# Performance work log

Measured on AMD Instinct MI355X. Metric: run time of the kernel, lower is better.

## Reference

```python
import jax, jax.numpy as jnp
import numpy as np
from jax import lax

RSM_K = 35
PFM_K = 31


def _box_sum(x, k):
    # Separable zero-padded box sum, equivalent to conv2d with a uniform kxk
    # kernel and padding=k//2 (odd k -> SAME). x: [B,1,H,W]
    p = k // 2
    pad = ((0, 0), (0, 0), (p, p), (0, 0))
    x = lax.reduce_window(x, 0.0, lax.add, (1, 1, k, 1), (1, 1, 1, 1), pad)
    pad = ((0, 0), (0, 0), (0, 0), (p, p))
    x = lax.reduce_window(x, 0.0, lax.add, (1, 1, 1, k), (1, 1, 1, 1), pad)
    return x


def _dilate(x, k):
    # Separable morphological dilation == max_pool2d(kernel=k, stride=1, pad=k//2).
    # -inf padding matches torch's max_pool2d padding semantics for 0/1 masks.
    p = k // 2
    ninf = -jnp.inf
    pad = ((0, 0), (0, 0), (p, p), (0, 0))
    x = lax.reduce_window(x, ninf, lax.max, (1, 1, k, 1), (1, 1, 1, 1), pad)
    pad = ((0, 0), (0, 0), (0, 0), (p, p))
    x = lax.reduce_window(x, ninf, lax.max, (1, 1, 1, k), (1, 1, 1, 1), pad)
    return x


def setup_inputs() -> dict:
    key = jax.random.key(0)
    # Sparse binary lesion mask, values exactly 0.0 / 1.0, shape [B,1,H,W]
    masks = (jax.random.uniform(key, (32, 1, 768, 768)) < 0.02).astype(jnp.float32)
    return {"masks": masks}


def reference(masks):
    # RSM: probability map = uniform 35x35 box average (conv2d with 1/k^2 kernel)
    rsm = _box_sum(masks, RSM_K) * (1.0 / (RSM_K * RSM_K))  # [B,1,H,W]
    # PFM: 1 = lesion, 0 = surrounding (inside 31x31 dilation), 2 = ignore
    dilated = _dilate(masks, PFM_K)
    pfm = jnp.where(masks > 0.5, 1, jnp.where(dilated > 0.5, 0, 2))
    pfm = pfm.astype(jnp.int32)[:, 0, :, :]  # [B,H,W]
    return rsm, pfm
```

## Files before the change

kernel.cpp:

```cpp
#include <hip/hip_runtime.h>


#define BATCH 32
#define HH 768
#define WW 768
#define NPIX (HH * WW)

constexpr int TYO  = 48;
constexpr int HALO = 17;
constexpr int ROWS = TYO + 2 * HALO;
constexpr int NSEG = 12;
constexpr int SSEG = NSEG + 2;
constexpr int NT   = 768;
constexpr int NG   = 4;
constexpr int RPG  = TYO / NG;
constexpr int CT   = 192;

typedef float v4f __attribute__((ext_vector_type(4)));

__global__ __launch_bounds__(NT)
void label_gen_fused(const float* __restrict__ in, float* __restrict__ out) {
    __shared__ unsigned long long sbits[ROWS][SSEG];
    __shared__ unsigned int hm[ROWS][CT];

    const int tid  = threadIdx.x;
    const int lane = tid & 63;
    const int wv   = tid >> 6;
    const int y0   = blockIdx.x * TYO;
    const int b    = blockIdx.y;
    const float* __restrict__ src = in + (size_t)b * NPIX;

    for (int lr = wv; lr < ROWS; lr += NT / 64) {
        const int r = y0 - HALO + lr;
        unsigned long long bb[NSEG];
        if ((unsigned)r < (unsigned)HH) {
            const float* rp = src + (size_t)r * WW;
            #pragma unroll
            for (int j = 0; j < NSEG; ++j)
                bb[j] = __ballot(rp[64 * j + lane] > 0.5f);
        } else {
            #pragma unroll
            for (int j = 0; j < NSEG; ++j) bb[j] = 0ull;
        }
        if (lane == 0) {
            sbits[lr][0] = 0ull;
            #pragma unroll
            for (int j = 0; j < NSEG; ++j) sbits[lr][j + 1] = bb[j];
            sbits[lr][SSEG - 1] = 0ull;
        }
    }
    __syncthreads();

    {
        const int r0 = tid / CT;
        const int ct = tid - r0 * CT;
        const int c0 = 4 * ct;
        const int s  = c0 - HALO;
        const int q  = (s >> 6) + 1;
        const int sh = s & 63;
        const unsigned long long M35 = (1ull << 35) - 1;
        for (int lr = r0; lr < ROWS; lr += NG) {
            const unsigned long long w =
                (sbits[lr][q] >> sh) | (sbits[lr][q + 1] << (64 - sh));
            const int h0 = (int)__popcll(w & M35);
            const int h1 = h0 + (int)((w >> 35) & 1) - (int)(w & 1);
            const int h2 = h1 + (int)((w >> 36) & 1) - (int)((w >> 1) & 1);
            const int h3 = h2 + (int)((w >> 37) & 1) - (int)((w >> 2) & 1);
            unsigned long long sm = w | (w >> 1);
            sm |= sm >> 2; sm |= sm >> 4; sm |= sm >> 8;
            const unsigned int o4 = (unsigned int)(((sm >> 2) | (sm >> 17)) & 0xFull);
            const unsigned int m4 = (unsigned int)((w >> 17) & 0xFull);
            const unsigned int mb =
                (((m4 & 1u) | ((m4 & 2u) << 7) | ((m4 & 4u) << 14) | ((m4 & 8u) << 21)) << 6);
            const unsigned int ob =
                (((o4 & 1u) | ((o4 & 2u) << 7) | ((o4 & 4u) << 14) | ((o4 & 8u) << 21)) << 7);
            hm[lr][ct] = (unsigned)h0 | ((unsigned)h1 << 8) | ((unsigned)h2 << 16)
                       | ((unsigned)h3 << 24) | mb | ob;
        }
    }
    __syncthreads();

    const int g   = tid / CT;
    const int ct  = tid - g * CT;
    const int c0  = 4 * ct;
    const int yb  = y0 + RPG * g;
    const int lr0 = RPG * g;

    const unsigned int M6 = 0x003F003Fu;
    const unsigned int M1 = 0x01010101u;

    unsigned int vA = 0, vB = 0;
    unsigned int c31 = 0;
    unsigned int ring_e[2], ring_l[2];
    #pragma unroll
    for (int k = 0; k < 35; ++k) {
        const unsigned int x = hm[lr0 + k][ct];
        vA += x & M6;
        vB += (x >> 8) & M6;
        if (k >= 2 && k <= 32) c31 += (x >> 7) & M1;
        if (k == 0)  ring_l[0] = x;
        if (k == 1)  ring_l[1] = x;
        if (k == 33) ring_e[0] = x;
        if (k == 34) ring_e[1] = x;
    }

    float* orow = out + (size_t)b * NPIX + (size_t)yb * WW + c0;
    float* prow = orow + (size_t)BATCH * NPIX;

    for (int i = 0; i < RPG; ++i) {
        const int lr = lr0 + HALO + i;
        const unsigned int xc = hm[lr][ct];

        v4f r4, p4;
        r4.x = (float)(vA & 0xFFFFu) * (1.0f / 1225.0f);
        r4.y = (float)(vB & 0xFFFFu) * (1.0f / 1225.0f);
        r4.z = (float)(vA >> 16)     * (1.0f / 1225.0f);
        r4.w = (float)(vB >> 16)     * (1.0f / 1225.0f);
        p4.x = ((xc >> 6) & 1u)  ? 1.0f : ((c31 & 0xFFu)         ? 0.0f : 2.0f);
        p4.y = ((xc >> 14) & 1u) ? 1.0f : (((c31 >> 8) & 0xFFu)  ? 0.0f : 2.0f);
        p4.z = ((xc >> 22) & 1u) ? 1.0f : (((c31 >> 16) & 0xFFu) ? 0.0f : 2.0f);
        p4.w = ((xc >> 30) & 1u) ? 1.0f : ((c31 >> 24)           ? 0.0f : 2.0f);

        __builtin_nontemporal_store(r4, (v4f*)orow);
        __builtin_nontemporal_store(p4, (v4f*)prow);
        orow += WW; prow += WW;

        if (i < RPG - 1) {
            const unsigned int xe   = hm[lr + 18][ct];
            const unsigned int xl31 = hm[lr0 + 2 + i][ct];
            const unsigned int xe31 = ring_e[i & 1];
            const unsigned int xl   = ring_l[i & 1];
            ring_e[i & 1] = xe;
            ring_l[i & 1] = xl31;
            vA  = (vA + (xe & M6)) - (xl & M6);
            vB  = (vB + ((xe >> 8) & M6)) - ((xl >> 8) & M6);
            c31 = (c31 + ((xe31 >> 7) & M1)) - ((xl31 >> 7) & M1);
        }
    }
}

extern "C" void kernel_launch(void* const* d_in, const int* in_sizes, int n_in,
                              void* d_out, int out_size, void* d_ws, size_t ws_size,
                              hipStream_t stream) {
    const float* masks = (const float*)d_in[0];
    float* out = (float*)d_out;
    dim3 grid(HH / TYO, BATCH);
    label_gen_fused<<<grid, NT, 0, stream>>>(masks, out);
}
```

Measured before the change: 211.7 us.

## Prepack mask to bitmap in a separate kernel to avoid halo float rereads

```diff
diff --git a/kernel.cpp b/kernel.cpp
--- a/kernel.cpp
+++ b/kernel.cpp
@@ -18,36 +18,44 @@
 
 typedef float v4f __attribute__((ext_vector_type(4)));
 
+__global__ __launch_bounds__(256)
+void packbits_kernel(const float* __restrict__ in,
+                     unsigned long long* __restrict__ bits) {
+    const int lane = threadIdx.x & 63;
+    const int wv   = threadIdx.x >> 6;
+    const size_t gr = (size_t)blockIdx.x * 4 + wv;
+    const float* rp = in + gr * WW;
+    unsigned long long bb = 0;
+    #pragma unroll
+    for (int j = 0; j < NSEG; ++j) {
+        const unsigned long long m = __ballot(rp[64 * j + lane] > 0.5f);
+        if (lane == j) bb = m;
+    }
+    if (lane < NSEG) bits[gr * NSEG + lane] = bb;
+}
+
 __global__ __launch_bounds__(NT)
-void label_gen_fused(const float* __restrict__ in, float* __restrict__ out) {
+void label_gen_fused_bits(const unsigned long long* __restrict__ bits,
+                          float* __restrict__ out) {
     __shared__ unsigned long long sbits[ROWS][SSEG];
     __shared__ unsigned int hm[ROWS][CT];
 
-    const int tid  = threadIdx.x;
-    const int lane = tid & 63;
-    const int wv   = tid >> 6;
-    const int y0   = blockIdx.x * TYO;
-    const int b    = blockIdx.y;
-    const float* __restrict__ src = in + (size_t)b * NPIX;
-
-    for (int lr = wv; lr < ROWS; lr += NT / 64) {
-        const int r = y0 - HALO + lr;
-        unsigned long long bb[NSEG];
-        if ((unsigned)r < (unsigned)HH) {
-            const float* rp = src + (size_t)r * WW;
-            #pragma unroll
-            for (int j = 0; j < NSEG; ++j)
-                bb[j] = __ballot(rp[64 * j + lane] > 0.5f);
-        } else {
-            #pragma unroll
-            for (int j = 0; j < NSEG; ++j) bb[j] = 0ull;
-        }
-        if (lane == 0) {
-            sbits[lr][0] = 0ull;
-            #pragma unroll
-            for (int j = 0; j < NSEG; ++j) sbits[lr][j + 1] = bb[j];
-            sbits[lr][SSEG - 1] = 0ull;
-        }
+    const int tid = threadIdx.x;
+    const int y0  = blockIdx.x * TYO;
+    const int b   = blockIdx.y;
+
+    for (int idx = tid; idx < ROWS * NSEG; idx += NT) {
+        const int lr = idx / NSEG;
+        const int j  = idx - lr * NSEG;
+        const int r  = y0 - HALO + lr;
+        unsigned long long v = 0ull;
+        if ((unsigned)r < (unsigned)HH)
+            v = bits[((size_t)b * HH + r) * NSEG + j];
+        sbits[lr][j + 1] = v;
+    }
+    for (int lr = tid; lr < ROWS; lr += NT) {
+        sbits[lr][0] = 0ull;
+        sbits[lr][SSEG - 1] = 0ull;
     }
     __syncthreads();
 
@@ -139,11 +147,135 @@
     }
 }
 
+__global__ __launch_bounds__(NT)
+void label_gen_fused(const float* __restrict__ in, float* __restrict__ out) {
+    __shared__ unsigned long long sbits[ROWS][SSEG];
+    __shared__ unsigned int hm[ROWS][CT];
+
+    const int tid  = threadIdx.x;
+    const int lane = tid & 63;
+    const int wv   = tid >> 6;
+    const int y0   = blockIdx.x * TYO;
+    const int b    = blockIdx.y;
+    const float* __restrict__ src = in + (size_t)b * NPIX;
+
+    for (int lr = wv; lr < ROWS; lr += NT / 64) {
+        const int r = y0 - HALO + lr;
+        unsigned long long bb[NSEG];
+        if ((unsigned)r < (unsigned)HH) {
+            const float* rp = src + (size_t)r * WW;
+            #pragma unroll
+            for (int j = 0; j < NSEG; ++j)
+                bb[j] = __ballot(rp[64 * j + lane] > 0.5f);
+        } else {
+            #pragma unroll
+            for (int j = 0; j < NSEG; ++j) bb[j] = 0ull;
+        }
+        if (lane == 0) {
+            sbits[lr][0] = 0ull;
+            #pragma unroll
+            for (int j = 0; j < NSEG; ++j) sbits[lr][j + 1] = bb[j];
+            sbits[lr][SSEG - 1] = 0ull;
+        }
+    }
+    __syncthreads();
+
+    {
+        const int r0 = tid / CT;
+        const int ct = tid - r0 * CT;
+        const int c0 = 4 * ct;
+        const int s  = c0 - HALO;
+        const int q  = (s >> 6) + 1;
+        const int sh = s & 63;
+        const unsigned long long M35 = (1ull << 35) - 1;
+        for (int lr = r0; lr < ROWS; lr += NG) {
+            const unsigned long long w =
+                (sbits[lr][q] >> sh) | (sbits[lr][q + 1] << (64 - sh));
+            const int h0 = (int)__popcll(w & M35);
+            const int h1 = h0 + (int)((w >> 35) & 1) - (int)(w & 1);
+            const int h2 = h1 + (int)((w >> 36) & 1) - (int)((w >> 1) & 1);
+            const int h3 = h2 + (int)((w >> 37) & 1) - (int)((w >> 2) & 1);
+            unsigned long long sm = w | (w >> 1);
+            sm |= sm >> 2; sm |= sm >> 4; sm |= sm >> 8;
+            const unsigned int o4 = (unsigned int)(((sm >> 2) | (sm >> 17)) & 0xFull);
+            const unsigned int m4 = (unsigned int)((w >> 17) & 0xFull);
+            const unsigned int mb =
+                (((m4 & 1u) | ((m4 & 2u) << 7) | ((m4 & 4u) << 14) | ((m4 & 8u) << 21)) << 6);
+            const unsigned int ob =
+                (((o4 & 1u) | ((o4 & 2u) << 7) | ((o4 & 4u) << 14) | ((o4 & 8u) << 21)) << 7);
+            hm[lr][ct] = (unsigned)h0 | ((unsigned)h1 << 8) | ((unsigned)h2 << 16)
+                       | ((unsigned)h3 << 24) | mb | ob;
+        }
+    }
+    __syncthreads();
+
+    const int g   = tid / CT;
+    const int ct  = tid - g * CT;
+    const int c0  = 4 * ct;
+    const int yb  = y0 + RPG * g;
+    const int lr0 = RPG * g;
+    const unsigned int M6 = 0x003F003Fu;
+    const unsigned int M1 = 0x01010101u;
+
+    unsigned int vA = 0, vB = 0, c31 = 0;
+    unsigned int ring_e[2], ring_l[2];
+    #pragma unroll
+    for (int k = 0; k < 35; ++k) {
+        const unsigned int x = hm[lr0 + k][ct];
+        vA += x & M6;
+        vB += (x >> 8) & M6;
+        if (k >= 2 && k <= 32) c31 += (x >> 7) & M1;
+        if (k == 0)  ring_l[0] = x;
+        if (k == 1)  ring_l[1] = x;
+        if (k == 33) ring_e[0] = x;
+        if (k == 34) ring_e[1] = x;
+    }
+
+    float* orow = out + (size_t)b * NPIX + (size_t)yb * WW + c0;
+    float* prow = orow + (size_t)BATCH * NPIX;
+
+    for (int i = 0; i < RPG; ++i) {
+        const int lr = lr0 + HALO + i;
+        const unsigned int xc = hm[lr][ct];
+        v4f r4, p4;
+        r4.x = (float)(vA & 0xFFFFu) * (1.0f / 1225.0f);
+        r4.y = (float)(vB & 0xFFFFu) * (1.0f / 1225.0f);
+        r4.z = (float)(vA >> 16)     * (1.0f / 1225.0f);
+        r4.w = (float)(vB >> 16)     * (1.0f / 1225.0f);
+        p4.x = ((xc >> 6) & 1u)  ? 1.0f : ((c31 & 0xFFu)         ? 0.0f : 2.0f);
+        p4.y = ((xc >> 14) & 1u) ? 1.0f : (((c31 >> 8) & 0xFFu)  ? 0.0f : 2.0f);
+        p4.z = ((xc >> 22) & 1u) ? 1.0f : (((c31 >> 16) & 0xFFu) ? 0.0f : 2.0f);
+        p4.w = ((xc >> 30) & 1u) ? 1.0f : ((c31 >> 24)           ? 0.0f : 2.0f);
+        __builtin_nontemporal_store(r4, (v4f*)orow);
+        __builtin_nontemporal_store(p4, (v4f*)prow);
+        orow += WW; prow += WW;
+        if (i < RPG - 1) {
+            const unsigned int xe   = hm[lr + 18][ct];
+            const unsigned int xl31 = hm[lr0 + 2 + i][ct];
+            const unsigned int xe31 = ring_e[i & 1];
+            const unsigned int xl   = ring_l[i & 1];
+            ring_e[i & 1] = xe;
+            ring_l[i & 1] = xl31;
+            vA  = (vA + (xe & M6)) - (xl & M6);
+            vB  = (vB + ((xe >> 8) & M6)) - ((xl >> 8) & M6);
+            c31 = (c31 + ((xe31 >> 7) & M1)) - ((xl31 >> 7) & M1);
+        }
+    }
+}
+
 extern "C" void kernel_launch(void* const* d_in, const int* in_sizes, int n_in,
                               void* d_out, int out_size, void* d_ws, size_t ws_size,
                               hipStream_t stream) {
     const float* masks = (const float*)d_in[0];
     float* out = (float*)d_out;
-    dim3 grid(HH / TYO, BATCH);
-    label_gen_fused<<<grid, NT, 0, stream>>>(masks, out);
-}
+    const size_t need = (size_t)BATCH * HH * NSEG * sizeof(unsigned long long);
+    if (ws_size >= need) {
+        unsigned long long* bitsmap = (unsigned long long*)d_ws;
+        packbits_kernel<<<dim3(BATCH * HH / 4), 256, 0, stream>>>(masks, bitsmap);
+        dim3 grid(HH / TYO, BATCH);
+        label_gen_fused_bits<<<grid, NT, 0, stream>>>(bitsmap, out);
+    } else {
+        dim3 grid(HH / TYO, BATCH);
+        label_gen_fused<<<grid, NT, 0, stream>>>(masks, out);
+    }
+}
```

Measured after the change: 211.7 us. About the same (+0.0%).
